# Optimization experiments

Measured on AMD Instinct MI355X. Metric: run time of the kernel, lower is better.

Reference implementation:

```python
import jax, jax.numpy as jnp
import numpy as np

NUM_HEADS = 8
ROPE_BASE = 10000.0


def _rope(x):
    # x: [B, S, E]; standard interleaved rotary embedding applied on full embed dim
    B, S, E = x.shape
    half = E // 2
    inv_freq = 1.0 / (ROPE_BASE ** (jnp.arange(0, half, dtype=jnp.float32) * 2.0 / E))
    freqs = jnp.arange(S, dtype=jnp.float32)[:, None] * inv_freq[None, :]  # [S, E/2]
    cos = jnp.cos(freqs)[None]  # [1, S, E/2]
    sin = jnp.sin(freqs)[None]
    x1 = x[..., 0::2]
    x2 = x[..., 1::2]
    r1 = x1 * cos - x2 * sin
    r2 = x1 * sin + x2 * cos
    return jnp.stack([r1, r2], axis=-1).reshape(B, S, E)


def setup_inputs() -> dict:
    key = jax.random.key(0)
    ks = jax.random.split(key, 7)
    B, S, E = 2, 4096, 512
    q = jax.random.normal(ks[0], (B, S, E), dtype=jnp.float32)
    k = jax.random.normal(ks[1], (B, S, E), dtype=jnp.float32)
    v = jax.random.normal(ks[2], (B, S, E), dtype=jnp.float32)
    scale = 1.0 / np.sqrt(E)
    in_proj_w = jax.random.normal(ks[3], (3 * E, E), dtype=jnp.float32) * scale
    in_proj_b = jnp.zeros((3 * E,), dtype=jnp.float32)
    out_proj_w = jax.random.normal(ks[4], (E, E), dtype=jnp.float32) * scale
    out_proj_b = jnp.zeros((E,), dtype=jnp.float32)
    return {"query": q, "key": k, "value": v,
            "in_proj_w": in_proj_w, "in_proj_b": in_proj_b,
            "out_proj_w": out_proj_w, "out_proj_b": out_proj_b}


def reference(query, key, value, in_proj_w, in_proj_b, out_proj_w, out_proj_b):
    B, S, E = query.shape
    H = NUM_HEADS
    D = E // H
    # RoPE applied before projection, as in the original module
    q_in = _rope(query)
    k_in = _rope(key)
    Wq, Wk, Wv = jnp.split(in_proj_w, 3, axis=0)
    bq, bk, bv = jnp.split(in_proj_b, 3, axis=0)
    q = (q_in @ Wq.T + bq).reshape(B, S, H, D).transpose(0, 2, 1, 3)  # [B,H,S,D]
    k = (k_in @ Wk.T + bk).reshape(B, S, H, D).transpose(0, 2, 1, 3)
    v = (value @ Wv.T + bv).reshape(B, S, H, D).transpose(0, 2, 1, 3)
    scores = jnp.einsum('bhqd,bhkd->bhqk', q, k) / jnp.sqrt(jnp.asarray(D, q.dtype))
    weights = jax.nn.softmax(scores, axis=-1)  # [B,H,S,S]
    ctx = jnp.einsum('bhqk,bhkd->bhqd', weights, v)  # [B,H,S,D]
    ctx = ctx.transpose(0, 2, 1, 3).reshape(B, S, E)
    attn_output = ctx @ out_proj_w.T + out_proj_b
    attn_weights = weights.mean(axis=1)  # averaged over heads (need_weights=True default)
    return attn_output, attn_weights
```

## Files before the change

### kernel.cpp

```cpp
#include <hip/hip_runtime.h>
#include <stdint.h>
#include <stddef.h>


#define B_ 2
#define S_ 4096
#define E_ 512
#define H_ 8
#define D_ 64
#define BS_ (B_*S_)

typedef __attribute__((ext_vector_type(8)))  short short8;
typedef __attribute__((ext_vector_type(4)))  float f32x4;
typedef __attribute__((ext_vector_type(16))) float f32x16;
typedef __attribute__((ext_vector_type(4)))  int   i32x4;

#define DEVFN static __device__ __forceinline__

DEVFN short f2bf(float x) {
    unsigned u = __builtin_bit_cast(unsigned, x);
    u += 0x7fffu + ((u >> 16) & 1u);
    return (short)(u >> 16);
}

__global__ void k_cstable(float2* __restrict__ cs) {
    int pos = blockIdx.x;
    int i   = threadIdx.x;
    double ang = (double)pos * exp(-0.035977892078031968 * (double)i);
    cs[pos * 256 + i] = make_float2((float)cos(ang), (float)sin(ang));
}

__global__ void k_rope(const float* __restrict__ x, const float2* __restrict__ cs,
                       short* __restrict__ out) {
    int row = blockIdx.x;
    int i   = threadIdx.x;
    int s   = row & (S_ - 1);
    float2 c = cs[s * 256 + i];
    float x1 = x[(size_t)row * E_ + 2 * i];
    float x2 = x[(size_t)row * E_ + 2 * i + 1];
    float r1 = x1 * c.x - x2 * c.y;
    float r2 = x1 * c.y + x2 * c.x;
    unsigned pk = ((unsigned)(unsigned short)f2bf(r1)) |
                  (((unsigned)(unsigned short)f2bf(r2)) << 16);
    *reinterpret_cast<unsigned*>(out + (size_t)row * E_ + 2 * i) = pk;
}

__global__ void k_cast8(const float* __restrict__ in, short* __restrict__ out, int n8) {
    int i = blockIdx.x * 256 + threadIdx.x;
    if (i < n8) {
        f32x4 a = *reinterpret_cast<const f32x4*>(in + (size_t)i * 8);
        f32x4 b = *reinterpret_cast<const f32x4*>(in + (size_t)i * 8 + 4);
        short8 o;
#pragma unroll
        for (int j = 0; j < 4; j++) { o[j] = f2bf(a[j]); o[4 + j] = f2bf(b[j]); }
        *reinterpret_cast<short8*>(out + (size_t)i * 8) = o;
    }
}

template<int MODE>
__global__ __launch_bounds__(256) void k_gemm_bt(
    const short* __restrict__ A, int K,
    const short* __restrict__ Bw,
    const float* __restrict__ bias,
    short* __restrict__ out_bf, float* __restrict__ out_f) {
    __shared__ short sA[128 * 72];
    __shared__ short sB[128 * 72];
    int tid = threadIdx.x;
    int lane = tid & 63, wv = tid >> 6;
    int lane16 = lane & 15, lgrp = lane >> 4;
    int row0 = blockIdx.y * 128;
    int col0 = blockIdx.x * 128;
    int wr = (wv >> 1) * 64, wc = (wv & 1) * 64;

    f32x4 acc[4][4];
#pragma unroll
    for (int i = 0; i < 4; i++)
#pragma unroll
        for (int j = 0; j < 4; j++)
#pragma unroll
            for (int r = 0; r < 4; r++) acc[i][j][r] = 0.f;

    int nk = K >> 6;
    for (int kt = 0; kt < nk; ++kt) {
        short8 va[4], vb[4];
#pragma unroll
        for (int i = 0; i < 4; i++) {
            int ch = i * 256 + tid;
            int r = ch >> 3, ce = (ch & 7) * 8;
            va[i] = *reinterpret_cast<const short8*>(A  + (size_t)(row0 + r) * K + kt * 64 + ce);
            vb[i] = *reinterpret_cast<const short8*>(Bw + (size_t)(col0 + r) * K + kt * 64 + ce);
        }
        __syncthreads();
#pragma unroll
        for (int i = 0; i < 4; i++) {
            int ch = i * 256 + tid;
            int r = ch >> 3, ce = (ch & 7) * 8;
            *reinterpret_cast<short8*>(sA + r * 72 + ce) = va[i];
            *reinterpret_cast<short8*>(sB + r * 72 + ce) = vb[i];
        }
        __syncthreads();
#pragma unroll
        for (int ks = 0; ks < 2; ++ks) {
            short8 af[4];
#pragma unroll
            for (int i = 0; i < 4; i++)
                af[i] = *reinterpret_cast<const short8*>(sA + (wr + i * 16 + lane16) * 72 + ks * 32 + lgrp * 8);
#pragma unroll
            for (int j = 0; j < 4; j++) {
                short8 bf = *reinterpret_cast<const short8*>(sB + (wc + j * 16 + lane16) * 72 + ks * 32 + lgrp * 8);
#pragma unroll
                for (int i = 0; i < 4; i++)
                    acc[i][j] = __builtin_amdgcn_mfma_f32_16x16x32_bf16(af[i], bf, acc[i][j], 0, 0, 0);
            }
        }
    }
#pragma unroll
    for (int i = 0; i < 4; i++) {
#pragma unroll
        for (int j = 0; j < 4; j++) {
            int col = col0 + wc + j * 16 + lane16;
            float bv = bias ? bias[col] : 0.f;
#pragma unroll
            for (int r = 0; r < 4; r++) {
                int row = row0 + wr + i * 16 + lgrp * 4 + r;
                float v = acc[i][j][r] + bv;
                if (MODE == 0 || MODE == 1) {
                    if (MODE == 0) v *= 0.18033688011112042f;
                    int b = row >> 12, s = row & (S_ - 1);
                    int h = col >> 6, d = col & 63;
                    out_bf[((size_t)(b * H_ + h) * S_ + s) * D_ + d] = f2bf(v);
                } else if (MODE == 2) {
                    out_bf[(size_t)row * E_ + col] = f2bf(v);
                } else {
                    out_f[(size_t)row * E_ + col] = v;
                }
            }
        }
    }
}

__global__ void k_transpose_v(const short* __restrict__ vin, short* __restrict__ Vt) {
    __shared__ short t[64][66];
    int bid = blockIdx.x;
    int st = bid & 63, h = (bid >> 6) & 7, b = bid >> 9;
    int tid = threadIdx.x;
#pragma unroll
    for (int i = 0; i < 16; i++) {
        int idx = i * 256 + tid;
        int sl = idx >> 6, d = idx & 63;
        t[sl][d] = vin[((size_t)(b * S_ + st * 64 + sl)) * E_ + h * 64 + d];
    }
    __syncthreads();
#pragma unroll
    for (int i = 0; i < 16; i++) {
        int idx = i * 256 + tid;
        int dl = idx >> 6, sl = idx & 63;
        Vt[((size_t)(b * H_ + h) * 64 + dl) * S_ + st * 64 + sl] = t[sl][dl];
    }
}

DEVFN short8 lds_rd(const short* buf, int row, int colb) {
    return *reinterpret_cast<const short8*>(
        (const char*)buf + row * 128 + (colb ^ ((row & 7) << 4)));
}

__global__ __launch_bounds__(256) void k_flash(
    const short* __restrict__ Qh, const short* __restrict__ Kh,
    const short* __restrict__ Vt, short* __restrict__ ctxb,
    float* __restrict__ Lrow) {
    __shared__ short kbuf[2][64 * 64];
    __shared__ short vbuf[2][64 * 64];
    __shared__ short ob[4][32 * 72];
    int tid = threadIdx.x, lane = tid & 63, wv = tid >> 6;
    int l31 = lane & 31, hi = lane >> 5;
    int gid = blockIdx.x;
    int qt = gid & 31, h = (gid >> 5) & 7, b = gid >> 8;
    int bh = b * H_ + h;
    int qrow0 = qt * 128 + wv * 32;
    const short* Qp = Qh + ((size_t)bh * S_ + qrow0) * D_;
    const short* Kp = Kh + (size_t)bh * S_ * D_;
    const short* Vp = Vt + (size_t)bh * 64 * S_;

    short8 qf[4];
#pragma unroll
    for (int ds = 0; ds < 4; ds++)
        qf[ds] = *reinterpret_cast<const short8*>(
            Qp + (size_t)l31 * D_ + ds * 16 + hi * 8);

    f32x16 ctx0, ctx1;
#pragma unroll
    for (int r = 0; r < 16; r++) { ctx0[r] = 0.f; ctx1[r] = 0.f; }
    float lsum = 0.f;

    int srow = wv * 16 + (lane >> 3);
    int scol = (lane & 7) * 8;
    int swz  = (scol * 2) ^ ((lane >> 3) << 4);

    short8 kst[2], vst[2];
#define STAGE_LOAD(kb_) do {                                                     \
    int nb_ = (kb_);                                                             \
    _Pragma("unroll") for (int ci = 0; ci < 2; ci++) {                           \
        int r_ = srow + ci * 8;                                                  \
        kst[ci] = *reinterpret_cast<const short8*>(Kp + (size_t)(nb_ + r_) * D_ + scol); \
        vst[ci] = *reinterpret_cast<const short8*>(Vp + (size_t)r_ * S_ + nb_ + scol);   \
    } } while (0)
#define STAGE_WRITE(d_) do {                                                     \
    _Pragma("unroll") for (int ci = 0; ci < 2; ci++) {                           \
        int r_ = srow + ci * 8;                                                  \
        *reinterpret_cast<short8*>((char*)kbuf[d_] + r_ * 128 + swz) = kst[ci];  \
        *reinterpret_cast<short8*>((char*)vbuf[d_] + r_ * 128 + swz) = vst[ci];  \
    } } while (0)

    STAGE_LOAD(0);
    STAGE_WRITE(0);
    __syncthreads();
    int cur = 0;

    for (int kt = 0; kt < 64; ++kt) {
        if (kt < 63) STAGE_LOAD((kt + 1) * 64);

        f32x16 s0, s1;
#pragma unroll
        for (int r = 0; r < 16; r++) { s0[r] = 0.f; s1[r] = 0.f; }
#pragma unroll
        for (int ds = 0; ds < 4; ds++) {
            short8 k0 = lds_rd(kbuf[cur], l31,      ds * 32 + hi * 16);
            short8 k1 = lds_rd(kbuf[cur], 32 + l31, ds * 32 + hi * 16);
            s0 = __builtin_amdgcn_mfma_f32_32x32x16_bf16(k0, qf[ds], s0, 0, 0, 0);
            s1 = __builtin_amdgcn_mfma_f32_32x32x16_bf16(k1, qf[ds], s1, 0, 0, 0);
        }
#pragma unroll
        for (int r = 0; r < 16; r++) { s0[r] = __builtin_amdgcn_exp2f(s0[r]); lsum += s0[r]; }
#pragma unroll
        for (int r = 0; r < 16; r++) { s1[r] = __builtin_amdgcn_exp2f(s1[r]); lsum += s1[r]; }

        int w[16];
#pragma unroll
        for (int t = 0; t < 8; t++) {
            asm("v_cvt_pk_bf16_f32 %0, %1, %2" : "=v"(w[t])     : "v"(s0[2 * t]), "v"(s0[2 * t + 1]));
            asm("v_cvt_pk_bf16_f32 %0, %1, %2" : "=v"(w[8 + t]) : "v"(s1[2 * t]), "v"(s1[2 * t + 1]));
        }
        short8 pf[4];
#pragma unroll
        for (int g = 0; g < 4; g++) {
            int a0 = w[g * 4 + 0], b0 = w[g * 4 + 2];
            int a1 = w[g * 4 + 1], b1 = w[g * 4 + 3];
            asm("v_permlane32_swap_b32 %0, %1" : "+v"(a0), "+v"(b0));
            asm("v_permlane32_swap_b32 %0, %1" : "+v"(a1), "+v"(b1));
            i32x4 t4 = {a0, a1, b0, b1};
            pf[g] = __builtin_bit_cast(short8, t4);
        }
#pragma unroll
        for (int ks = 0; ks < 4; ks++) {
            short8 v0 = lds_rd(vbuf[cur], l31,      ks * 32 + hi * 16);
            short8 v1 = lds_rd(vbuf[cur], 32 + l31, ks * 32 + hi * 16);
            ctx0 = __builtin_amdgcn_mfma_f32_32x32x16_bf16(v0, pf[ks], ctx0, 0, 0, 0);
            ctx1 = __builtin_amdgcn_mfma_f32_32x32x16_bf16(v1, pf[ks], ctx1, 0, 0, 0);
        }
        if (kt < 63) STAGE_WRITE(cur ^ 1);
        __syncthreads();
        cur ^= 1;
    }

    float l_run = lsum + __shfl_xor(lsum, 32);
    float invl = 1.0f / l_run;
    short* obw = &ob[wv][0];
#pragma unroll
    for (int n = 0; n < 2; n++) {
#pragma unroll
        for (int t = 0; t < 8; t++) {
            float a  = (n ? ctx1[2 * t]     : ctx0[2 * t])     * invl;
            float bb = (n ? ctx1[2 * t + 1] : ctx0[2 * t + 1]) * invl;
            int wd;
            asm("v_cvt_pk_bf16_f32 %0, %1, %2" : "=v"(wd) : "v"(a), "v"(bb));
            int d = n * 32 + ((2 * t) & 3) + 8 * ((2 * t) >> 2) + 4 * hi;
            *reinterpret_cast<int*>(obw + l31 * 72 + d) = wd;
        }
    }
    __syncthreads();
    {
        int q = lane >> 1, half = lane & 1;
        size_t gbase = ((size_t)b * S_ + qrow0 + q) * E_ + h * 64 + half * 32;
#pragma unroll
        for (int j = 0; j < 4; j++) {
            short8 vvv = *reinterpret_cast<const short8*>(obw + q * 72 + half * 32 + j * 8);
            *reinterpret_cast<short8*>(ctxb + gbase + j * 8) = vvv;
        }
    }
    if (lane < 32)
        Lrow[(size_t)bh * S_ + qrow0 + lane] = l_run;
#undef STAGE_LOAD
#undef STAGE_WRITE
}

__global__ __launch_bounds__(256) void k_weights(
    const short* __restrict__ Qh, const short* __restrict__ Kh,
    const float* __restrict__ Lrow,
    float* __restrict__ outw) {
    __shared__ short Kt[2][64 * 64];
    __shared__ short Qt[2][128 * 64];
    __shared__ float c_lds[1024];
    int tid = threadIdx.x, lane = tid & 63, wv = tid >> 6;
    int l31 = lane & 31, hi = lane >> 5;
    int gid = blockIdx.x;
    int kc = gid & 63, qt = (gid >> 6) & 31, b = gid >> 11;
    int k0 = kc * 64;
    int qblk = qt * 128;
    int qrow0 = qblk + wv * 32;

    {
        int e0 = tid * 4;
        int hh = e0 >> 7, qq = e0 & 127;
        size_t base = ((size_t)(b * H_ + hh)) * S_ + qblk + qq;
        f32x4 lv = *reinterpret_cast<const f32x4*>(&Lrow[base]);
        f32x4 cc;
#pragma unroll
        for (int j = 0; j < 4; j++) cc[j] = -3.0f - __log2f(lv[j]);
        *reinterpret_cast<f32x4*>(&c_lds[e0]) = cc;
    }

    int srow8 = lane >> 3;
    int scol  = (lane & 7) * 8;
    int swz   = (scol * 2) ^ (srow8 << 4);

    const short* Kbase = Kh + ((size_t)(b * H_) * S_ + k0) * D_;
    const short* Qbase = Qh + ((size_t)(b * H_) * S_ + qblk) * D_;

    short8 kst[2], qst[4];
#pragma unroll
    for (int ci = 0; ci < 2; ci++)
        kst[ci] = *reinterpret_cast<const short8*>(
            Kbase + (size_t)(wv * 16 + ci * 8 + srow8) * D_ + scol);
#pragma unroll
    for (int ci = 0; ci < 4; ci++)
        qst[ci] = *reinterpret_cast<const short8*>(
            Qbase + (size_t)(wv * 32 + ci * 8 + srow8) * D_ + scol);
#pragma unroll
    for (int ci = 0; ci < 2; ci++)
        *reinterpret_cast<short8*>((char*)Kt[0] + (wv * 16 + ci * 8 + srow8) * 128 + swz) = kst[ci];
#pragma unroll
    for (int ci = 0; ci < 4; ci++)
        *reinterpret_cast<short8*>((char*)Qt[0] + (wv * 32 + ci * 8 + srow8) * 128 + swz) = qst[ci];
    __syncthreads();

    f32x16 w0, w1;
#pragma unroll
    for (int r = 0; r < 16; r++) { w0[r] = 0.f; w1[r] = 0.f; }

    int cur = 0;
    for (int h = 0; h < H_; ++h) {
        if (h < 7) {
            const short* kp = Kbase + (size_t)(h + 1) * S_ * D_;
            const short* qp = Qbase + (size_t)(h + 1) * S_ * D_;
#pragma unroll
            for (int ci = 0; ci < 2; ci++)
                kst[ci] = *reinterpret_cast<const short8*>(
                    kp + (size_t)(wv * 16 + ci * 8 + srow8) * D_ + scol);
#pragma unroll
            for (int ci = 0; ci < 4; ci++)
                qst[ci] = *reinterpret_cast<const short8*>(
                    qp + (size_t)(wv * 32 + ci * 8 + srow8) * D_ + scol);
        }
        f32x16 s0, s1;
#pragma unroll
        for (int g = 0; g < 4; g++) {
            f32x4 ci4 = *reinterpret_cast<const f32x4*>(
                &c_lds[h * 128 + wv * 32 + 4 * hi + 8 * g]);
#pragma unroll
            for (int j = 0; j < 4; j++) { s0[g * 4 + j] = ci4[j]; s1[g * 4 + j] = ci4[j]; }
        }
#pragma unroll
        for (int ks = 0; ks < 4; ks++) {
            short8 aq = lds_rd(Qt[cur], wv * 32 + l31, ks * 32 + hi * 16);
            short8 b0 = lds_rd(Kt[cur], l31,           ks * 32 + hi * 16);
            short8 b1 = lds_rd(Kt[cur], 32 + l31,      ks * 32 + hi * 16);
            s0 = __builtin_amdgcn_mfma_f32_32x32x16_bf16(aq, b0, s0, 0, 0, 0);
            s1 = __builtin_amdgcn_mfma_f32_32x32x16_bf16(aq, b1, s1, 0, 0, 0);
        }
#pragma unroll
        for (int r = 0; r < 16; r++) {
            w0[r] += __builtin_amdgcn_exp2f(s0[r]);
            w1[r] += __builtin_amdgcn_exp2f(s1[r]);
        }
        if (h < 7) {
#pragma unroll
            for (int ci = 0; ci < 2; ci++)
                *reinterpret_cast<short8*>((char*)Kt[cur ^ 1] + (wv * 16 + ci * 8 + srow8) * 128 + swz) = kst[ci];
#pragma unroll
            for (int ci = 0; ci < 4; ci++)
                *reinterpret_cast<short8*>((char*)Qt[cur ^ 1] + (wv * 32 + ci * 8 + srow8) * 128 + swz) = qst[ci];
        }
        __syncthreads();
        cur ^= 1;
    }
#pragma unroll
    for (int r = 0; r < 16; r++) {
        int qrow = qrow0 + (r & 3) + 8 * (r >> 2) + 4 * hi;
        float* op = outw + ((size_t)b * S_ + qrow) * (size_t)S_ + k0;
        op[l31]      = w0[r];
        op[32 + l31] = w1[r];
    }
}

extern "C" void kernel_launch(void* const* d_in, const int* in_sizes, int n_in,
                              void* d_out, int out_size, void* d_ws, size_t ws_size,
                              hipStream_t stream) {
    (void)in_sizes; (void)n_in; (void)out_size; (void)ws_size;
    const float* q     = (const float*)d_in[0];
    const float* k     = (const float*)d_in[1];
    const float* v     = (const float*)d_in[2];
    const float* in_w  = (const float*)d_in[3];
    const float* in_b  = (const float*)d_in[4];
    const float* out_w = (const float*)d_in[5];
    const float* out_b = (const float*)d_in[6];
    float* out  = (float*)d_out;
    float* outw = out + (size_t)B_ * S_ * E_;

    char* ws = (char*)d_ws;
    size_t off = 0;
    auto alloc = [&](size_t bytes) { void* p = ws + off; off += (bytes + 255) & ~(size_t)255; return p; };

    float2* cs   = (float2*)alloc((size_t)S_ * 256 * 8);
    short*  Aq   = (short*) alloc((size_t)BS_ * E_ * 2);
    short*  Ak   = (short*) alloc((size_t)BS_ * E_ * 2);
    short*  Av   = (short*) alloc((size_t)BS_ * E_ * 2);
    short*  Wall = (short*) alloc((size_t)3 * E_ * E_ * 2);
    short*  Wo   = (short*) alloc((size_t)E_ * E_ * 2);
    short*  Qh   = (short*) alloc((size_t)B_ * H_ * S_ * D_ * 2);
    short*  Kh   = (short*) alloc((size_t)B_ * H_ * S_ * D_ * 2);
    short*  vtmp = (short*) alloc((size_t)BS_ * E_ * 2);
    short*  Vt   = (short*) alloc((size_t)B_ * H_ * D_ * S_ * 2);
    short*  ctxb = (short*) alloc((size_t)BS_ * E_ * 2);
    float*  Lrow = (float*) alloc((size_t)B_ * H_ * S_ * 4);

    k_cstable<<<S_, 256, 0, stream>>>(cs);
    k_rope<<<BS_, 256, 0, stream>>>(q, cs, Aq);
    k_rope<<<BS_, 256, 0, stream>>>(k, cs, Ak);
    k_cast8<<<(BS_ * E_ / 8 + 255) / 256, 256, 0, stream>>>(v, Av, BS_ * E_ / 8);
    k_cast8<<<(3 * E_ * E_ / 8 + 255) / 256, 256, 0, stream>>>(in_w, Wall, 3 * E_ * E_ / 8);
    k_cast8<<<(E_ * E_ / 8 + 255) / 256, 256, 0, stream>>>(out_w, Wo, E_ * E_ / 8);

    dim3 gg(E_ / 128, BS_ / 128);
    k_gemm_bt<0><<<gg, 256, 0, stream>>>(Aq, E_, Wall,             in_b,        Qh,   nullptr);
    k_gemm_bt<1><<<gg, 256, 0, stream>>>(Ak, E_, Wall + E_ * E_,   in_b + E_,   Kh,   nullptr);
    k_gemm_bt<2><<<gg, 256, 0, stream>>>(Av, E_, Wall + 2 * E_ * E_, in_b + 2 * E_, vtmp, nullptr);
    k_transpose_v<<<B_ * H_ * (S_ / 64), 256, 0, stream>>>(vtmp, Vt);
    k_flash<<<B_ * H_ * (S_ / 128), 256, 0, stream>>>(Qh, Kh, Vt, ctxb, Lrow);
    k_gemm_bt<3><<<gg, 256, 0, stream>>>(ctxb, E_, Wo, out_b, nullptr, out);
    k_weights<<<B_ * (S_ / 128) * (S_ / 64), 256, 0, stream>>>(Qh, Kh, Lrow, outw);
}
```

Before: 263.7 us.

## Split flash attention over key halves and combine partials in a new kernel

The flash kernel now splits the key range into two halves, doubling the grid from 512 to 1024 blocks. Each block writes unnormalized bf16 partial context and its partial row sum, and a new combine kernel sums the two halves and normalizes. The aim is more parallelism on the many CUs. The cost is an extra kernel launch, extra global traffic for the partials, and an extra bf16 rounding. k_weights also drops Q double buffering to cut LDS use, adding a barrier.

Measured after the change: 271.0 us. 1.03x slower.

```diff
diff --git a/kernel.cpp b/kernel.cpp
--- a/kernel.cpp
+++ b/kernel.cpp
@@ -9,6 +9,7 @@
 #define H_ 8
 #define D_ 64
 #define BS_ (B_*S_)
+#define BHS_ (B_*H_*S_)
 
 typedef __attribute__((ext_vector_type(8)))  short short8;
 typedef __attribute__((ext_vector_type(4)))  float f32x4;
@@ -21,6 +22,10 @@
     unsigned u = __builtin_bit_cast(unsigned, x);
     u += 0x7fffu + ((u >> 16) & 1u);
     return (short)(u >> 16);
+}
+DEVFN float bf2f(short s) {
+    unsigned u = ((unsigned)(unsigned short)s) << 16;
+    return __builtin_bit_cast(float, u);
 }
 
 __global__ void k_cstable(float2* __restrict__ cs) {
@@ -166,17 +171,18 @@
 
 __global__ __launch_bounds__(256) void k_flash(
     const short* __restrict__ Qh, const short* __restrict__ Kh,
-    const short* __restrict__ Vt, short* __restrict__ ctxb,
-    float* __restrict__ Lrow) {
-    __shared__ short kbuf[2][64 * 64];
-    __shared__ short vbuf[2][64 * 64];
-    __shared__ short ob[4][32 * 72];
+    const short* __restrict__ Vt, short* __restrict__ Cp,
+    float* __restrict__ Lp) {
+    __shared__ short smem[4][64 * 64];
+    short (*kbuf)[64 * 64] = &smem[0];
+    short (*vbuf)[64 * 64] = &smem[2];
     int tid = threadIdx.x, lane = tid & 63, wv = tid >> 6;
     int l31 = lane & 31, hi = lane >> 5;
     int gid = blockIdx.x;
-    int qt = gid & 31, h = (gid >> 5) & 7, b = gid >> 8;
+    int split = gid & 1, qt = (gid >> 1) & 31, h = (gid >> 6) & 7, b = gid >> 9;
     int bh = b * H_ + h;
     int qrow0 = qt * 128 + wv * 32;
+    int kbase0 = split * 2048;
     const short* Qp = Qh + ((size_t)bh * S_ + qrow0) * D_;
     const short* Kp = Kh + (size_t)bh * S_ * D_;
     const short* Vp = Vt + (size_t)bh * 64 * S_;
@@ -211,13 +217,13 @@
         *reinterpret_cast<short8*>((char*)vbuf[d_] + r_ * 128 + swz) = vst[ci];  \
     } } while (0)
 
-    STAGE_LOAD(0);
+    STAGE_LOAD(kbase0);
     STAGE_WRITE(0);
     __syncthreads();
     int cur = 0;
 
-    for (int kt = 0; kt < 64; ++kt) {
-        if (kt < 63) STAGE_LOAD((kt + 1) * 64);
+    for (int kt = 0; kt < 32; ++kt) {
+        if (kt < 31) STAGE_LOAD(kbase0 + (kt + 1) * 64);
 
         f32x16 s0, s1;
 #pragma unroll
@@ -257,20 +263,19 @@
             ctx0 = __builtin_amdgcn_mfma_f32_32x32x16_bf16(v0, pf[ks], ctx0, 0, 0, 0);
             ctx1 = __builtin_amdgcn_mfma_f32_32x32x16_bf16(v1, pf[ks], ctx1, 0, 0, 0);
         }
-        if (kt < 63) STAGE_WRITE(cur ^ 1);
+        if (kt < 31) STAGE_WRITE(cur ^ 1);
         __syncthreads();
         cur ^= 1;
     }
 
     float l_run = lsum + __shfl_xor(lsum, 32);
-    float invl = 1.0f / l_run;
-    short* obw = &ob[wv][0];
+    short* obw = (short*)smem + wv * (32 * 72);
 #pragma unroll
     for (int n = 0; n < 2; n++) {
 #pragma unroll
         for (int t = 0; t < 8; t++) {
-            float a  = (n ? ctx1[2 * t]     : ctx0[2 * t])     * invl;
-            float bb = (n ? ctx1[2 * t + 1] : ctx0[2 * t + 1]) * invl;
+            float a  = (n ? ctx1[2 * t]     : ctx0[2 * t]);
+            float bb = (n ? ctx1[2 * t + 1] : ctx0[2 * t + 1]);
             int wd;
             asm("v_cvt_pk_bf16_f32 %0, %1, %2" : "=v"(wd) : "v"(a), "v"(bb));
             int d = n * 32 + ((2 * t) & 3) + 8 * ((2 * t) >> 2) + 4 * hi;
@@ -279,26 +284,46 @@
     }
     __syncthreads();
     {
+        short* Cpp = Cp + (size_t)split * BS_ * E_;
         int q = lane >> 1, half = lane & 1;
         size_t gbase = ((size_t)b * S_ + qrow0 + q) * E_ + h * 64 + half * 32;
 #pragma unroll
         for (int j = 0; j < 4; j++) {
             short8 vvv = *reinterpret_cast<const short8*>(obw + q * 72 + half * 32 + j * 8);
-            *reinterpret_cast<short8*>(ctxb + gbase + j * 8) = vvv;
+            *reinterpret_cast<short8*>(Cpp + gbase + j * 8) = vvv;
         }
     }
     if (lane < 32)
-        Lrow[(size_t)bh * S_ + qrow0 + lane] = l_run;
+        Lp[(size_t)split * BHS_ + (size_t)bh * S_ + qrow0 + lane] = l_run;
 #undef STAGE_LOAD
 #undef STAGE_WRITE
 }
 
+__global__ __launch_bounds__(256) void k_combine(
+    const short* __restrict__ Cp, const float* __restrict__ Lp,
+    short* __restrict__ ctxb) {
+    int i8 = blockIdx.x * 256 + threadIdx.x;
+    size_t e0 = (size_t)i8 * 8;
+    int row = (int)(e0 >> 9);
+    int col = (int)(e0 & 511);
+    int b = row >> 12, s = row & (S_ - 1), h = col >> 6;
+    size_t lidx = (size_t)(b * H_ + h) * S_ + s;
+    float invl = 1.0f / (Lp[lidx] + Lp[BHS_ + lidx]);
+    short8 c0 = *reinterpret_cast<const short8*>(Cp + e0);
+    short8 c1 = *reinterpret_cast<const short8*>(Cp + (size_t)BS_ * E_ + e0);
+    short8 o;
+#pragma unroll
+    for (int j = 0; j < 8; j++)
+        o[j] = f2bf((bf2f(c0[j]) + bf2f(c1[j])) * invl);
+    *reinterpret_cast<short8*>(ctxb + e0) = o;
+}
+
 __global__ __launch_bounds__(256) void k_weights(
     const short* __restrict__ Qh, const short* __restrict__ Kh,
-    const float* __restrict__ Lrow,
+    const float* __restrict__ Lp,
     float* __restrict__ outw) {
     __shared__ short Kt[2][64 * 64];
-    __shared__ short Qt[2][128 * 64];
+    __shared__ short Qt[128 * 64];
     __shared__ float c_lds[1024];
     int tid = threadIdx.x, lane = tid & 63, wv = tid >> 6;
     int l31 = lane & 31, hi = lane >> 5;
@@ -312,10 +337,11 @@
         int e0 = tid * 4;
         int hh = e0 >> 7, qq = e0 & 127;
         size_t base = ((size_t)(b * H_ + hh)) * S_ + qblk + qq;
-        f32x4 lv = *reinterpret_cast<const f32x4*>(&Lrow[base]);
+        f32x4 lv0 = *reinterpret_cast<const f32x4*>(&Lp[base]);
+        f32x4 lv1 = *reinterpret_cast<const f32x4*>(&Lp[BHS_ + base]);
         f32x4 cc;
 #pragma unroll
-        for (int j = 0; j < 4; j++) cc[j] = -3.0f - __log2f(lv[j]);
+        for (int j = 0; j < 4; j++) cc[j] = -3.0f - __log2f(lv0[j] + lv1[j]);
         *reinterpret_cast<f32x4*>(&c_lds[e0]) = cc;
     }
 
@@ -340,7 +366,7 @@
         *reinterpret_cast<short8*>((char*)Kt[0] + (wv * 16 + ci * 8 + srow8) * 128 + swz) = kst[ci];
 #pragma unroll
     for (int ci = 0; ci < 4; ci++)
-        *reinterpret_cast<short8*>((char*)Qt[0] + (wv * 32 + ci * 8 + srow8) * 128 + swz) = qst[ci];
+        *reinterpret_cast<short8*>((char*)Qt + (wv * 32 + ci * 8 + srow8) * 128 + swz) = qst[ci];
     __syncthreads();
 
     f32x16 w0, w1;
@@ -371,7 +397,7 @@
         }
 #pragma unroll
         for (int ks = 0; ks < 4; ks++) {
-            short8 aq = lds_rd(Qt[cur], wv * 32 + l31, ks * 32 + hi * 16);
+            short8 aq = lds_rd(Qt, wv * 32 + l31,      ks * 32 + hi * 16);
             short8 b0 = lds_rd(Kt[cur], l31,           ks * 32 + hi * 16);
             short8 b1 = lds_rd(Kt[cur], 32 + l31,      ks * 32 + hi * 16);
             s0 = __builtin_amdgcn_mfma_f32_32x32x16_bf16(aq, b0, s0, 0, 0, 0);
@@ -382,13 +408,14 @@
             w0[r] += __builtin_amdgcn_exp2f(s0[r]);
             w1[r] += __builtin_amdgcn_exp2f(s1[r]);
         }
+        __syncthreads();
         if (h < 7) {
 #pragma unroll
             for (int ci = 0; ci < 2; ci++)
                 *reinterpret_cast<short8*>((char*)Kt[cur ^ 1] + (wv * 16 + ci * 8 + srow8) * 128 + swz) = kst[ci];
 #pragma unroll
             for (int ci = 0; ci < 4; ci++)
-                *reinterpret_cast<short8*>((char*)Qt[cur ^ 1] + (wv * 32 + ci * 8 + srow8) * 128 + swz) = qst[ci];
+                *reinterpret_cast<short8*>((char*)Qt + (wv * 32 + ci * 8 + srow8) * 128 + swz) = qst[ci];
         }
         __syncthreads();
         cur ^= 1;
@@ -431,7 +458,8 @@
     short*  vtmp = (short*) alloc((size_t)BS_ * E_ * 2);
     short*  Vt   = (short*) alloc((size_t)B_ * H_ * D_ * S_ * 2);
     short*  ctxb = (short*) alloc((size_t)BS_ * E_ * 2);
-    float*  Lrow = (float*) alloc((size_t)B_ * H_ * S_ * 4);
+    short*  Cp   = (short*) alloc((size_t)2 * BS_ * E_ * 2);
+    float*  Lp   = (float*) alloc((size_t)2 * BHS_ * 4);
 
     k_cstable<<<S_, 256, 0, stream>>>(cs);
     k_rope<<<BS_, 256, 0, stream>>>(q, cs, Aq);
@@ -445,7 +473,8 @@
     k_gemm_bt<1><<<gg, 256, 0, stream>>>(Ak, E_, Wall + E_ * E_,   in_b + E_,   Kh,   nullptr);
     k_gemm_bt<2><<<gg, 256, 0, stream>>>(Av, E_, Wall + 2 * E_ * E_, in_b + 2 * E_, vtmp, nullptr);
     k_transpose_v<<<B_ * H_ * (S_ / 64), 256, 0, stream>>>(vtmp, Vt);
-    k_flash<<<B_ * H_ * (S_ / 128), 256, 0, stream>>>(Qh, Kh, Vt, ctxb, Lrow);
+    k_flash<<<B_ * H_ * (S_ / 128) * 2, 256, 0, stream>>>(Qh, Kh, Vt, Cp, Lp);
+    k_combine<<<(BS_ * E_ / 8) / 256, 256, 0, stream>>>(Cp, Lp, ctxb);
     k_gemm_bt<3><<<gg, 256, 0, stream>>>(ctxb, E_, Wo, out_b, nullptr, out);
-    k_weights<<<B_ * (S_ / 128) * (S_ / 64), 256, 0, stream>>>(Qh, Kh, Lrow, outw);
-}
+    k_weights<<<B_ * (S_ / 128) * (S_ / 64), 256, 0, stream>>>(Qh, Kh, Lp, outw);
+}
```
